# Kernel optimization log

Hardware: AMD Instinct MI355X
Metric: run time of the kernel (lower is better)

The kernel has to match this reference:

```python
import jax, jax.numpy as jnp
import numpy as np

B, M, N = 8, 8192, 8192  # batch, input neurons, output neurons
SPIKE_CAP = 0.9          # VPRTempo caps spike amplitude at 0.9


def setup_inputs() -> dict:
    key = jax.random.key(0)
    k0, k1, k2, k3 = jax.random.split(key, 4)
    # pre-synaptic spike amplitudes in [0, 1)
    pre_spikes = jax.random.uniform(k0, (B, 1, M), dtype=jnp.float32)
    # combined excitatory+inhibitory weights
    W = jax.random.normal(k1, (M, N), dtype=jnp.float32) * 0.01
    # per-neuron thresholds, uniform in thr_range = [0, 0.5]
    thr = jax.random.uniform(k2, (B, 1, N), dtype=jnp.float32) * 0.5
    # per-neuron constant input, uniform in const_inp = [0, 0.1]
    const_inp = jax.random.uniform(k3, (B, 1, N), dtype=jnp.float32) * 0.1
    return {"pre_spikes": pre_spikes, "W": W, "thr": thr, "const_inp": const_inp}


def reference(pre_spikes, W, thr, const_inp):
    # membrane potential: weighted pre-synaptic spikes + constant input
    x = jnp.einsum('bom,mn->bon', pre_spikes, W) + const_inp  # [B,1,N]
    # spike generation: amplitude above threshold, clamped to [0, 0.9]
    spikes = jnp.clip(x - thr, 0.0, SPIKE_CAP)
    return spikes
```

## Files before the change

kernel.cpp:

```cpp
#include <hip/hip_runtime.h>


constexpr int Mdim = 8192;
constexpr int Ndim = 8192;
constexpr int Bdim = 8;
constexpr int PANELS  = 8;
constexpr int PANEL_N = Ndim / PANELS;
constexpr int CHUNKS  = 64;
constexpr int CROWS   = Mdim / CHUNKS;
constexpr float CAP = 0.9f;

__global__ __launch_bounds__(256, 2) void snn_stage1(
    const float* __restrict__ pre,
    const float* __restrict__ W,
    float* __restrict__ part)
{
    __shared__ float lds_pre[Bdim * CROWS];

    const int t     = threadIdx.x;
    const int panel = blockIdx.x;
    const int chunk = blockIdx.y;
    const int r0    = chunk * CROWS;
    const int col   = panel * PANEL_N + t * 4;

#pragma unroll
    for (int q = t; q < Bdim * CROWS; q += 256) {
        int b = q >> 7, j = q & 127;
        lds_pre[q] = pre[b * Mdim + r0 + j];
    }

    float4 acc[Bdim];
#pragma unroll
    for (int b = 0; b < Bdim; ++b) acc[b] = make_float4(0.f, 0.f, 0.f, 0.f);

    const float* wcol = W + col;
    const int phase = (chunk * 5 + panel * 11) & 15;
    auto rowoff = [&](int i) { return ((i + phase) & 15) * 8; };

    auto loadW = [&](float4* w, int rr) {
        const float* base = wcol + (size_t)(r0 + rr) * Ndim;
#pragma unroll
        for (int j = 0; j < 8; ++j)
            w[j] = *reinterpret_cast<const float4*>(base + (size_t)j * Ndim);
    };

    auto compute = [&](const float4* w, int rr) {
#pragma unroll
        for (int half = 0; half < 2; ++half) {
            const float4 w0 = w[4 * half], w1 = w[4 * half + 1],
                         w2 = w[4 * half + 2], w3 = w[4 * half + 3];
#pragma unroll
            for (int b = 0; b < Bdim; ++b) {
                float4 p = *reinterpret_cast<const float4*>(
                    lds_pre + b * CROWS + rr + 4 * half);
                float4 a = acc[b];
                a.x = fmaf(p.x, w0.x, a.x); a.y = fmaf(p.x, w0.y, a.y);
                a.z = fmaf(p.x, w0.z, a.z); a.w = fmaf(p.x, w0.w, a.w);
                a.x = fmaf(p.y, w1.x, a.x); a.y = fmaf(p.y, w1.y, a.y);
                a.z = fmaf(p.y, w1.z, a.z); a.w = fmaf(p.y, w1.w, a.w);
                a.x = fmaf(p.z, w2.x, a.x); a.y = fmaf(p.z, w2.y, a.y);
                a.z = fmaf(p.z, w2.z, a.z); a.w = fmaf(p.z, w2.w, a.w);
                a.x = fmaf(p.w, w3.x, a.x); a.y = fmaf(p.w, w3.y, a.y);
                a.z = fmaf(p.w, w3.z, a.z); a.w = fmaf(p.w, w3.w, a.w);
                acc[b] = a;
            }
        }
    };

    float4 wa[8], wb[8];
    loadW(wa, rowoff(0));
    __syncthreads();

#pragma unroll
    for (int ii = 0; ii < 8; ++ii) {
        loadW(wb, rowoff(2 * ii + 1));
        compute(wa, rowoff(2 * ii));
        if (ii < 7) loadW(wa, rowoff(2 * ii + 2));
        compute(wb, rowoff(2 * ii + 1));
    }

    float* ps = part + (size_t)chunk * (Bdim * Ndim);
#pragma unroll
    for (int b = 0; b < Bdim; ++b)
        *reinterpret_cast<float4*>(ps + (size_t)b * Ndim + col) = acc[b];
}

__global__ __launch_bounds__(256, 4) void snn_stage2(
    const float* __restrict__ part,
    const float* __restrict__ thr,
    const float* __restrict__ cst,
    float* __restrict__ out)
{
    const int bid = blockIdx.x;
    const int i = bid * 256 + threadIdx.x;
    float s = 0.f;
#pragma unroll 8
    for (int k = 0; k < CHUNKS; ++k) {
        int kk = (k + bid * 7) & (CHUNKS - 1);
        s += part[(size_t)kk * (Bdim * Ndim) + i];
    }
    float x = s + cst[i] - thr[i];
    x = fminf(fmaxf(x, 0.f), CAP);
    out[i] = x;
}

extern "C" void kernel_launch(void* const* d_in, const int* in_sizes, int n_in,
                              void* d_out, int out_size, void* d_ws, size_t ws_size,
                              hipStream_t stream) {
    const float* pre = (const float*)d_in[0];
    const float* W   = (const float*)d_in[1];
    const float* thr = (const float*)d_in[2];
    const float* cst = (const float*)d_in[3];
    float* out  = (float*)d_out;
    float* part = (float*)d_ws;

    dim3 g1(PANELS, CHUNKS);
    hipLaunchKernelGGL(snn_stage1, g1, dim3(256), 0, stream, pre, W, part);

    dim3 g2((Bdim * Ndim) / 256);
    hipLaunchKernelGGL(snn_stage2, g2, dim3(256), 0, stream, part, thr, cst, out);
}
```

Before: 362.0 us.

## Split reduction over 256 row slabs with each block covering all columns

Measured after the change: 386.1 us. +6.7%, slower.

```diff
diff --git a/kernel.cpp b/kernel.cpp
--- a/kernel.cpp
+++ b/kernel.cpp
@@ -4,85 +4,75 @@
 constexpr int Mdim = 8192;
 constexpr int Ndim = 8192;
 constexpr int Bdim = 8;
-constexpr int PANELS  = 8;
-constexpr int PANEL_N = Ndim / PANELS;
-constexpr int CHUNKS  = 64;
-constexpr int CROWS   = Mdim / CHUNKS;
+constexpr int NBLK = 256;
+constexpr int SLAB = Mdim / NBLK;
 constexpr float CAP = 0.9f;
 
-__global__ __launch_bounds__(256, 2) void snn_stage1(
+__global__ __launch_bounds__(512, 2) void snn_stage1(
     const float* __restrict__ pre,
     const float* __restrict__ W,
     float* __restrict__ part)
 {
-    __shared__ float lds_pre[Bdim * CROWS];
+    __shared__ float lds_pre[Bdim * SLAB];
 
-    const int t     = threadIdx.x;
-    const int panel = blockIdx.x;
-    const int chunk = blockIdx.y;
-    const int r0    = chunk * CROWS;
-    const int col   = panel * PANEL_N + t * 4;
+    const int t  = threadIdx.x;
+    const int k  = blockIdx.x;
+    const int r0 = k * SLAB;
+    const int c0 = t * 4;
 
-#pragma unroll
-    for (int q = t; q < Bdim * CROWS; q += 256) {
-        int b = q >> 7, j = q & 127;
-        lds_pre[q] = pre[b * Mdim + r0 + j];
+    if (t < Bdim * SLAB) {
+        int b = t >> 5, j = t & (SLAB - 1);
+        lds_pre[t] = pre[b * Mdim + r0 + j];
     }
 
-    float4 acc[Bdim];
+    float4 acc[Bdim][4];
 #pragma unroll
-    for (int b = 0; b < Bdim; ++b) acc[b] = make_float4(0.f, 0.f, 0.f, 0.f);
+    for (int b = 0; b < Bdim; ++b)
+#pragma unroll
+        for (int j = 0; j < 4; ++j) acc[b][j] = make_float4(0.f, 0.f, 0.f, 0.f);
 
-    const float* wcol = W + col;
-    const int phase = (chunk * 5 + panel * 11) & 15;
-    auto rowoff = [&](int i) { return ((i + phase) & 15) * 8; };
+    const float* Wb = W + (size_t)r0 * Ndim + c0;
 
     auto loadW = [&](float4* w, int rr) {
-        const float* base = wcol + (size_t)(r0 + rr) * Ndim;
+        const float* p = Wb + (size_t)rr * Ndim;
 #pragma unroll
-        for (int j = 0; j < 8; ++j)
-            w[j] = *reinterpret_cast<const float4*>(base + (size_t)j * Ndim);
+        for (int j = 0; j < 4; ++j)
+            w[j] = *reinterpret_cast<const float4*>(p + 2048 * j);
     };
 
     auto compute = [&](const float4* w, int rr) {
 #pragma unroll
-        for (int half = 0; half < 2; ++half) {
-            const float4 w0 = w[4 * half], w1 = w[4 * half + 1],
-                         w2 = w[4 * half + 2], w3 = w[4 * half + 3];
+        for (int b = 0; b < Bdim; ++b) {
+            const float p = lds_pre[b * SLAB + rr];
 #pragma unroll
-            for (int b = 0; b < Bdim; ++b) {
-                float4 p = *reinterpret_cast<const float4*>(
-                    lds_pre + b * CROWS + rr + 4 * half);
-                float4 a = acc[b];
-                a.x = fmaf(p.x, w0.x, a.x); a.y = fmaf(p.x, w0.y, a.y);
-                a.z = fmaf(p.x, w0.z, a.z); a.w = fmaf(p.x, w0.w, a.w);
-                a.x = fmaf(p.y, w1.x, a.x); a.y = fmaf(p.y, w1.y, a.y);
-                a.z = fmaf(p.y, w1.z, a.z); a.w = fmaf(p.y, w1.w, a.w);
-                a.x = fmaf(p.z, w2.x, a.x); a.y = fmaf(p.z, w2.y, a.y);
-                a.z = fmaf(p.z, w2.z, a.z); a.w = fmaf(p.z, w2.w, a.w);
-                a.x = fmaf(p.w, w3.x, a.x); a.y = fmaf(p.w, w3.y, a.y);
-                a.z = fmaf(p.w, w3.z, a.z); a.w = fmaf(p.w, w3.w, a.w);
-                acc[b] = a;
+            for (int j = 0; j < 4; ++j) {
+                float4 a = acc[b][j];
+                a.x = fmaf(p, w[j].x, a.x);
+                a.y = fmaf(p, w[j].y, a.y);
+                a.z = fmaf(p, w[j].z, a.z);
+                a.w = fmaf(p, w[j].w, a.w);
+                acc[b][j] = a;
             }
         }
     };
 
-    float4 wa[8], wb[8];
-    loadW(wa, rowoff(0));
+    float4 wA[4], wB[4];
+    loadW(wA, 0);
     __syncthreads();
 
-#pragma unroll
-    for (int ii = 0; ii < 8; ++ii) {
-        loadW(wb, rowoff(2 * ii + 1));
-        compute(wa, rowoff(2 * ii));
-        if (ii < 7) loadW(wa, rowoff(2 * ii + 2));
-        compute(wb, rowoff(2 * ii + 1));
+    for (int rr = 0; rr < SLAB; rr += 2) {
+        loadW(wB, rr + 1);
+        compute(wA, rr);
+        if (rr + 2 < SLAB) loadW(wA, rr + 2);
+        compute(wB, rr + 1);
     }
 
-    float* ps = part + (size_t)chunk * (Bdim * Ndim);
+    float* ps = part + (size_t)k * (Bdim * Ndim) + c0;
 #pragma unroll
     for (int b = 0; b < Bdim; ++b)
-        *reinterpret_cast<float4*>(ps + (size_t)b * Ndim + col) = acc[b];
+#pragma unroll
+        for (int j = 0; j < 4; ++j)
+            *reinterpret_cast<float4*>(ps + (size_t)b * Ndim + 2048 * j) = acc[b][j];
 }
 
 __global__ __launch_bounds__(256, 4) void snn_stage2(
@@ -95,8 +85,8 @@
     const int i = bid * 256 + threadIdx.x;
     float s = 0.f;
 #pragma unroll 8
-    for (int k = 0; k < CHUNKS; ++k) {
-        int kk = (k + bid * 7) & (CHUNKS - 1);
+    for (int k = 0; k < NBLK; ++k) {
+        int kk = (k + bid) & (NBLK - 1);
         s += part[(size_t)kk * (Bdim * Ndim) + i];
     }
     float x = s + cst[i] - thr[i];
@@ -114,9 +104,7 @@
     float* out  = (float*)d_out;
     float* part = (float*)d_ws;
 
-    dim3 g1(PANELS, CHUNKS);
-    hipLaunchKernelGGL(snn_stage1, g1, dim3(256), 0, stream, pre, W, part);
-
-    dim3 g2((Bdim * Ndim) / 256);
-    hipLaunchKernelGGL(snn_stage2, g2, dim3(256), 0, stream, part, thr, cst, out);
+    hipLaunchKernelGGL(snn_stage1, dim3(NBLK), dim3(512), 0, stream, pre, W, part);
+    hipLaunchKernelGGL(snn_stage2, dim3((Bdim * Ndim) / 256), dim3(256), 0, stream,
+                       part, thr, cst, out);
 }
```
